# Performance work log

Hardware: AMD Instinct MI355X
Metric: run time of the kernel (lower is better)

The kernel has to match this reference:

```python
import jax, jax.numpy as jnp
import numpy as np

N_HEADS = 8
NUM_TIME_STEPS = 17  # T = NUM_TIME_STEPS - 1 = 16
MASK_PAD = np.float32(-2**32 + 1)


def setup_inputs() -> dict:
    key = jax.random.key(0)
    ks = jax.random.split(key, 5)
    B, T, D = 32768, NUM_TIME_STEPS - 1, 128
    return {
        "inputs": jax.random.normal(ks[0], (B, T, D), dtype=jnp.float32),
        "pos_emb": jax.random.normal(ks[1], (NUM_TIME_STEPS, D), dtype=jnp.float32) * 0.1,
        "Wq": jax.random.normal(ks[2], (D, D), dtype=jnp.float32) * (1.0 / np.sqrt(D)),
        "Wk": jax.random.normal(ks[3], (D, D), dtype=jnp.float32) * (1.0 / np.sqrt(D)),
        "Wv": jax.random.normal(ks[4], (D, D), dtype=jnp.float32) * (1.0 / np.sqrt(D)),
    }


def reference(inputs, pos_emb, Wq, Wk, Wv):
    B, T, D = inputs.shape
    h = N_HEADS
    dh = Wq.shape[1] // h
    # add positional embeddings for the first T time steps
    x = inputs + pos_emb[:T][None, :, :]  # [B, T, D]
    # QKV projections, then split into heads (torch.split dim=2 + cat dim=0 == head-major [h, B, T, dh])
    def proj(W):
        return jnp.einsum("btd,de->bte", x, W).reshape(B, T, h, dh).transpose(2, 0, 1, 3)
    q, k, v = proj(Wq), proj(Wk), proj(Wv)  # each [h, B, T, dh]
    # scaled scores; NOTE: original scales by sqrt(num_time_steps), not sqrt(head_dim)
    scores = jnp.einsum("hbtd,hbsd->hbts", q, k) / jnp.float32(NUM_TIME_STEPS) ** 0.5
    # causal mask: masked positions set to -2**32+1 (finite pad, as in the original)
    causal = jnp.tril(jnp.ones((T, T), dtype=bool))
    scores = jnp.where(causal[None, None, :, :], scores, MASK_PAD)
    attn = jax.nn.softmax(scores, axis=-1)  # [h, B, T, T]
    o = jnp.einsum("hbts,hbsd->hbtd", attn, v)  # [h, B, T, dh]
    # re-concat heads along feature dim (split dim0 + cat dim2)
    o = o.transpose(1, 2, 0, 3).reshape(B, T, h * dh)
    # feedforward: relu(x) + x
    o = jax.nn.relu(o) + o
    # residual=True: concat with temporal (position-added) inputs along features
    return jnp.concatenate([o, x], axis=2)  # [B, T, output_dim + input_dim]
```

## Files before the change

### kernel.cpp

```cpp
#include <hip/hip_runtime.h>

typedef float    f32x4 __attribute__((ext_vector_type(4)));
typedef __bf16   bf16x8 __attribute__((ext_vector_type(8)));
typedef _Float16 f16x4 __attribute__((ext_vector_type(4)));

typedef __attribute__((address_space(1))) const void gas_void;
typedef __attribute__((address_space(3))) void las_void;

static __device__ __forceinline__ unsigned short f2bf(float f) {
  union { float f; unsigned int u; } a; a.f = f;
  unsigned int r = (a.u + 0x7FFFu + ((a.u >> 16) & 1u)) >> 16;
  return (unsigned short)r;
}

#define QSCALE_L2E 0.34992146f

__global__ void prep_weights(const float* __restrict__ Wq, const float* __restrict__ Wk,
                             const float* __restrict__ Wv, unsigned short* __restrict__ wf) {
  int idx = blockIdx.x * 256 + threadIdx.x;
  if (idx >= 3 * 8 * 4 * 64 * 8) return;
  int i  = idx & 7;
  int p  = (idx >> 3) & 63;
  int kk = (idx >> 9) & 3;
  int n  = (idx >> 11) & 7;
  int w  = idx >> 14;
  const float* W = (w == 0) ? Wq : ((w == 1) ? Wk : Wv);
  float val = W[(kk * 32 + (p >> 4) * 8 + i) * 128 + n * 16 + (p & 15)];
  if (w == 0) val *= QSCALE_L2E;
  wf[idx] = f2bf(val);
}

__global__ void prep_posw(const float* __restrict__ pos, const float* __restrict__ Wq,
                          const float* __restrict__ Wk, const float* __restrict__ Wv,
                          float* __restrict__ pw) {
  int idx = blockIdx.x * 256 + threadIdx.x;
  if (idx >= 3 * 8 * 64 * 4) return;
  int r = idx & 3;
  int l = (idx >> 2) & 63;
  int h = (idx >> 8) & 7;
  int w = idx >> 11;
  const float* W = (w == 0) ? Wq : ((w == 1) ? Wk : Wv);
  int t, d;
  if (w < 2) { t = l & 15;            d = h * 16 + (l >> 4) * 4 + r; }
  else       { t = (l >> 4) * 4 + r;  d = h * 16 + (l & 15); }
  float s = 0.f;
  for (int k = 0; k < 128; ++k) s += pos[t * 128 + k] * W[k * 128 + d];
  if (w == 0) s *= QSCALE_L2E;
  pw[idx] = s;
}

__global__ void __launch_bounds__(512, 4)
attn_main(const float* __restrict__ xin, const float* __restrict__ pos,
          const unsigned short* __restrict__ wfrag, const float* __restrict__ pw,
          float* __restrict__ out, int B) {
  __shared__ __align__(16) float lx[2][4][2048];

  const int tid   = threadIdx.x;
  const int wid   = tid >> 6;
  const int l     = tid & 63;
  const int frow  = l & 15;
  const int fkq   = l >> 4;
  const int trow0 = fkq * 4;

  bf16x8 wf[3][4];
#pragma unroll
  for (int w = 0; w < 3; ++w)
#pragma unroll
    for (int kk = 0; kk < 4; ++kk)
      wf[w][kk] = *(const bf16x8*)(wfrag + ((w * 32 + wid * 4 + kk) * 512) + l * 8);

  f32x4 posw[3];
#pragma unroll
  for (int w = 0; w < 3; ++w)
    posw[w] = *(const f32x4*)(pw + ((w * 8 + wid) * 64 + l) * 4);

  const int ptcol = wid * 16 + fkq * 4;
  const f32x4 pp = *(const f32x4*)(pos + frow * 128 + ptcol);
  const int q    = 4 * wid + fkq;
  const int ptIdx = (((q >> 3) << 1) | (q & 1)) * 256 + (((q & 7) >> 1) * 16 + frow) * 4;

  const f32x4 zero4 = {0.f, 0.f, 0.f, 0.f};

  const int bpi   = gridDim.x * 4;
  const int niter = B / bpi;
  const int gsb   = frow * 128 + fkq * 8;
  const int bw    = wid >> 1;
  const int c0    = (wid & 1) * 4;

  {
    const float* xb = xin + (size_t)(blockIdx.x * 4 + bw) * 2048;
#pragma unroll
    for (int j = 0; j < 4; ++j) {
      int c = c0 + j;
      __builtin_amdgcn_global_load_lds((gas_void*)(xb + gsb + (c >> 1) * 32 + (c & 1) * 4),
                                       (las_void*)&lx[0][bw][c * 256], 16, 0, 0);
    }
  }
  int buf = 0;

  for (int it = 0; it < niter; ++it) {
    const int b0 = blockIdx.x * 4 + it * bpi;

    if (it == 0) {
      __syncthreads();
    } else {
      asm volatile("s_waitcnt vmcnt(8)" ::: "memory");
      __builtin_amdgcn_s_barrier();
    }

    if (it + 1 < niter) {
      const float* xb2 = xin + (size_t)(b0 + bpi + bw) * 2048;
#pragma unroll
      for (int j = 0; j < 4; ++j) {
        int c = c0 + j;
        __builtin_amdgcn_global_load_lds((gas_void*)(xb2 + gsb + (c >> 1) * 32 + (c & 1) * 4),
                                         (las_void*)&lx[buf ^ 1][bw][c * 256], 16, 0, 0);
      }
    }
    asm volatile("" ::: "memory");

#pragma unroll
    for (int g = 0; g < 4; ++g) {
      const float* lb = &lx[buf][g][0];
      float* ob = out + (size_t)(b0 + g) * 4096;

      bf16x8 xf[4];
#pragma unroll
      for (int kk = 0; kk < 4; ++kk) {
        f32x4 a0 = *(const f32x4*)(lb + (2 * kk + 0) * 256 + l * 4);
        f32x4 a1 = *(const f32x4*)(lb + (2 * kk + 1) * 256 + l * 4);
        xf[kk][0] = (__bf16)a0.x; xf[kk][1] = (__bf16)a0.y;
        xf[kk][2] = (__bf16)a0.z; xf[kk][3] = (__bf16)a0.w;
        xf[kk][4] = (__bf16)a1.x; xf[kk][5] = (__bf16)a1.y;
        xf[kk][6] = (__bf16)a1.z; xf[kk][7] = (__bf16)a1.w;
      }
      {
        f32x4 c0v = *(const f32x4*)(lb + ptIdx);
        *(f32x4*)(ob + frow * 256 + 128 + ptcol) = c0v + pp;
      }

      f32x4 qa = posw[0], ka = posw[1], va = posw[2];
#pragma unroll
      for (int kk = 0; kk < 4; ++kk) {
        qa = __builtin_amdgcn_mfma_f32_16x16x32_bf16(wf[0][kk], xf[kk], qa, 0, 0, 0);
        ka = __builtin_amdgcn_mfma_f32_16x16x32_bf16(wf[1][kk], xf[kk], ka, 0, 0, 0);
        va = __builtin_amdgcn_mfma_f32_16x16x32_bf16(xf[kk], wf[2][kk], va, 0, 0, 0);
      }
      f16x4 qh, kh, vh;
#pragma unroll
      for (int r = 0; r < 4; ++r) {
        qh[r] = (_Float16)qa[r];
        kh[r] = (_Float16)ka[r];
        vh[r] = (_Float16)va[r];
      }

      f32x4 st = __builtin_amdgcn_mfma_f32_16x16x16f16(kh, qh, zero4, 0, 0, 0);
      float p0 = (trow0 + 0 <= frow) ? __builtin_amdgcn_exp2f(st[0]) : 0.f;
      float p1 = (trow0 + 1 <= frow) ? __builtin_amdgcn_exp2f(st[1]) : 0.f;
      float p2 = (trow0 + 2 <= frow) ? __builtin_amdgcn_exp2f(st[2]) : 0.f;
      float p3 = (trow0 + 3 <= frow) ? __builtin_amdgcn_exp2f(st[3]) : 0.f;
      float ssum = (p0 + p1) + (p2 + p3);
      ssum += __shfl_xor(ssum, 16);
      ssum += __shfl_xor(ssum, 32);
      float inv = __builtin_amdgcn_rcpf(ssum);
      f16x4 ah;
      ah[0] = (_Float16)(p0 * inv);
      ah[1] = (_Float16)(p1 * inv);
      ah[2] = (_Float16)(p2 * inv);
      ah[3] = (_Float16)(p3 * inv);

      f32x4 ot = __builtin_amdgcn_mfma_f32_16x16x16f16(vh, ah, zero4, 0, 0, 0);
      f32x4 ov;
#pragma unroll
      for (int r = 0; r < 4; ++r) {
        float x = ot[r];
        ov[r] = x > 0.f ? 2.f * x : x;
      }
      *(f32x4*)(ob + frow * 256 + wid * 16 + trow0) = ov;
    }

    buf ^= 1;
  }
}

extern "C" void kernel_launch(void* const* d_in, const int* in_sizes, int n_in,
                              void* d_out, int out_size, void* d_ws, size_t ws_size,
                              hipStream_t stream) {
  (void)n_in; (void)out_size; (void)ws_size;
  const float* xin = (const float*)d_in[0];
  const float* pos = (const float*)d_in[1];
  const float* Wq  = (const float*)d_in[2];
  const float* Wk  = (const float*)d_in[3];
  const float* Wv  = (const float*)d_in[4];
  float* out = (float*)d_out;
  unsigned short* wf = (unsigned short*)d_ws;
  float* pw = (float*)((char*)d_ws + 3 * 8 * 4 * 64 * 8 * sizeof(unsigned short));
  int B = in_sizes[0] / 2048;

  hipLaunchKernelGGL(prep_weights, dim3(192), dim3(256), 0, stream, Wq, Wk, Wv, wf);
  hipLaunchKernelGGL(prep_posw, dim3(24), dim3(256), 0, stream, pos, Wq, Wk, Wv, pw);
  hipLaunchKernelGGL(attn_main, dim3(512), dim3(512), 0, stream, xin, pos, wf, pw, out, B);
}
```

Before: 176.2 us.

## Stage position-added bf16 inputs in LDS once and drop pos-projection prep kernel

Each wave now converts only its slice of the staged fp32 inputs, adds the positional embedding, and writes bf16 fragments into a double-buffered LDS array. The MFMA fragments are then read directly from that array, so the eight waves no longer each repeat the fp32-to-bf16 conversion for every batch element. The positional projection is now folded into the input before the QKV matmul, which removes the prep_posw kernel launch. The cost is that the residual x output is reconstructed from bf16-rounded values, so that half of the output loses precision. The fp32 staging buffer is also now single-buffered behind an extra LDS wait.

Result: faster. 170.2 us (-3.4%).

```diff
diff --git a/kernel.cpp b/kernel.cpp
--- a/kernel.cpp
+++ b/kernel.cpp
@@ -3,6 +3,7 @@
 typedef float    f32x4 __attribute__((ext_vector_type(4)));
 typedef __bf16   bf16x8 __attribute__((ext_vector_type(8)));
 typedef _Float16 f16x4 __attribute__((ext_vector_type(4)));
+typedef unsigned int u32x2 __attribute__((ext_vector_type(2)));
 
 typedef __attribute__((address_space(1))) const void gas_void;
 typedef __attribute__((address_space(3))) void las_void;
@@ -11,6 +12,9 @@
   union { float f; unsigned int u; } a; a.f = f;
   unsigned int r = (a.u + 0x7FFFu + ((a.u >> 16) & 1u)) >> 16;
   return (unsigned short)r;
+}
+static __device__ __forceinline__ float bits2f(unsigned int u) {
+  union { unsigned int u; float f; } a; a.u = u; return a.f;
 }
 
 #define QSCALE_L2E 0.34992146f
@@ -30,30 +34,11 @@
   wf[idx] = f2bf(val);
 }
 
-__global__ void prep_posw(const float* __restrict__ pos, const float* __restrict__ Wq,
-                          const float* __restrict__ Wk, const float* __restrict__ Wv,
-                          float* __restrict__ pw) {
-  int idx = blockIdx.x * 256 + threadIdx.x;
-  if (idx >= 3 * 8 * 64 * 4) return;
-  int r = idx & 3;
-  int l = (idx >> 2) & 63;
-  int h = (idx >> 8) & 7;
-  int w = idx >> 11;
-  const float* W = (w == 0) ? Wq : ((w == 1) ? Wk : Wv);
-  int t, d;
-  if (w < 2) { t = l & 15;            d = h * 16 + (l >> 4) * 4 + r; }
-  else       { t = (l >> 4) * 4 + r;  d = h * 16 + (l & 15); }
-  float s = 0.f;
-  for (int k = 0; k < 128; ++k) s += pos[t * 128 + k] * W[k * 128 + d];
-  if (w == 0) s *= QSCALE_L2E;
-  pw[idx] = s;
-}
-
 __global__ void __launch_bounds__(512, 4)
 attn_main(const float* __restrict__ xin, const float* __restrict__ pos,
-          const unsigned short* __restrict__ wfrag, const float* __restrict__ pw,
-          float* __restrict__ out, int B) {
-  __shared__ __align__(16) float lx[2][4][2048];
+          const unsigned short* __restrict__ wfrag, float* __restrict__ out, int B) {
+  __shared__ __align__(16) float lx[4][8][256];
+  __shared__ __align__(16) unsigned short lxb[2][4][4][512];
 
   const int tid   = threadIdx.x;
   const int wid   = tid >> 6;
@@ -69,23 +54,25 @@
     for (int kk = 0; kk < 4; ++kk)
       wf[w][kk] = *(const bf16x8*)(wfrag + ((w * 32 + wid * 4 + kk) * 512) + l * 8);
 
-  f32x4 posw[3];
+  const int bw = wid >> 1;
+  const int c0 = (wid & 1) * 4;
+
+  f32x4 posc[4];
 #pragma unroll
-  for (int w = 0; w < 3; ++w)
-    posw[w] = *(const f32x4*)(pw + ((w * 8 + wid) * 64 + l) * 4);
+  for (int cc = 0; cc < 4; ++cc) {
+    int c = c0 + cc;
+    posc[cc] = *(const f32x4*)(pos + frow * 128 + fkq * 8 + (c >> 1) * 32 + (c & 1) * 4);
+  }
 
   const int ptcol = wid * 16 + fkq * 4;
-  const f32x4 pp = *(const f32x4*)(pos + frow * 128 + ptcol);
-  const int q    = 4 * wid + fkq;
-  const int ptIdx = (((q >> 3) << 1) | (q & 1)) * 256 + (((q & 7) >> 1) * 16 + frow) * 4;
+  const int ptkk  = wid >> 1;
+  const int ptl   = frow + ((wid & 1) * 2 + (fkq >> 1)) * 16;
+  const int ptu   = ptl * 8 + (fkq & 1) * 4;
 
   const f32x4 zero4 = {0.f, 0.f, 0.f, 0.f};
-
   const int bpi   = gridDim.x * 4;
   const int niter = B / bpi;
   const int gsb   = frow * 128 + fkq * 8;
-  const int bw    = wid >> 1;
-  const int c0    = (wid & 1) * 4;
 
   {
     const float* xb = xin + (size_t)(blockIdx.x * 4 + bw) * 2048;
@@ -93,7 +80,7 @@
     for (int j = 0; j < 4; ++j) {
       int c = c0 + j;
       __builtin_amdgcn_global_load_lds((gas_void*)(xb + gsb + (c >> 1) * 32 + (c & 1) * 4),
-                                       (las_void*)&lx[0][bw][c * 256], 16, 0, 0);
+                                       (las_void*)&lx[bw][c][0], 16, 0, 0);
     }
   }
   int buf = 0;
@@ -101,12 +88,22 @@
   for (int it = 0; it < niter; ++it) {
     const int b0 = blockIdx.x * 4 + it * bpi;
 
-    if (it == 0) {
-      __syncthreads();
-    } else {
-      asm volatile("s_waitcnt vmcnt(8)" ::: "memory");
-      __builtin_amdgcn_s_barrier();
+    if (it == 0) asm volatile("s_waitcnt vmcnt(0)" ::: "memory");
+    else         asm volatile("s_waitcnt vmcnt(8)" ::: "memory");
+
+#pragma unroll
+    for (int i = 0; i < 2; ++i) {
+      int ce = c0 + 2 * i;
+      int kk = ce >> 1;
+      f32x4 a0 = *(const f32x4*)&lx[bw][ce][l * 4]     + posc[2 * i];
+      f32x4 a1 = *(const f32x4*)&lx[bw][ce + 1][l * 4] + posc[2 * i + 1];
+      bf16x8 v;
+      v[0] = (__bf16)a0.x; v[1] = (__bf16)a0.y; v[2] = (__bf16)a0.z; v[3] = (__bf16)a0.w;
+      v[4] = (__bf16)a1.x; v[5] = (__bf16)a1.y; v[6] = (__bf16)a1.z; v[7] = (__bf16)a1.w;
+      *(bf16x8*)&lxb[buf][bw][kk][l * 8] = v;
     }
+    asm volatile("s_waitcnt lgkmcnt(0)" ::: "memory");
+    __builtin_amdgcn_s_barrier();
 
     if (it + 1 < niter) {
       const float* xb2 = xin + (size_t)(b0 + bpi + bw) * 2048;
@@ -114,32 +111,31 @@
       for (int j = 0; j < 4; ++j) {
         int c = c0 + j;
         __builtin_amdgcn_global_load_lds((gas_void*)(xb2 + gsb + (c >> 1) * 32 + (c & 1) * 4),
-                                         (las_void*)&lx[buf ^ 1][bw][c * 256], 16, 0, 0);
+                                         (las_void*)&lx[bw][c][0], 16, 0, 0);
       }
     }
     asm volatile("" ::: "memory");
 
 #pragma unroll
     for (int g = 0; g < 4; ++g) {
-      const float* lb = &lx[buf][g][0];
       float* ob = out + (size_t)(b0 + g) * 4096;
 
       bf16x8 xf[4];
 #pragma unroll
-      for (int kk = 0; kk < 4; ++kk) {
-        f32x4 a0 = *(const f32x4*)(lb + (2 * kk + 0) * 256 + l * 4);
-        f32x4 a1 = *(const f32x4*)(lb + (2 * kk + 1) * 256 + l * 4);
-        xf[kk][0] = (__bf16)a0.x; xf[kk][1] = (__bf16)a0.y;
-        xf[kk][2] = (__bf16)a0.z; xf[kk][3] = (__bf16)a0.w;
-        xf[kk][4] = (__bf16)a1.x; xf[kk][5] = (__bf16)a1.y;
-        xf[kk][6] = (__bf16)a1.z; xf[kk][7] = (__bf16)a1.w;
-      }
+      for (int kk = 0; kk < 4; ++kk)
+        xf[kk] = *(const bf16x8*)&lxb[buf][g][kk][l * 8];
+
       {
-        f32x4 c0v = *(const f32x4*)(lb + ptIdx);
-        *(f32x4*)(ob + frow * 256 + 128 + ptcol) = c0v + pp;
+        u32x2 pv = *(const u32x2*)&lxb[buf][g][ptkk][ptu];
+        f32x4 ptv;
+        ptv.x = bits2f(pv[0] << 16);
+        ptv.y = bits2f(pv[0] & 0xffff0000u);
+        ptv.z = bits2f(pv[1] << 16);
+        ptv.w = bits2f(pv[1] & 0xffff0000u);
+        *(f32x4*)(ob + frow * 256 + 128 + ptcol) = ptv;
       }
 
-      f32x4 qa = posw[0], ka = posw[1], va = posw[2];
+      f32x4 qa = zero4, ka = zero4, va = zero4;
 #pragma unroll
       for (int kk = 0; kk < 4; ++kk) {
         qa = __builtin_amdgcn_mfma_f32_16x16x32_bf16(wf[0][kk], xf[kk], qa, 0, 0, 0);
@@ -194,10 +190,8 @@
   const float* Wv  = (const float*)d_in[4];
   float* out = (float*)d_out;
   unsigned short* wf = (unsigned short*)d_ws;
-  float* pw = (float*)((char*)d_ws + 3 * 8 * 4 * 64 * 8 * sizeof(unsigned short));
   int B = in_sizes[0] / 2048;
 
   hipLaunchKernelGGL(prep_weights, dim3(192), dim3(256), 0, stream, Wq, Wk, Wv, wf);
-  hipLaunchKernelGGL(prep_posw, dim3(24), dim3(256), 0, stream, pos, Wq, Wk, Wv, pw);
-  hipLaunchKernelGGL(attn_main, dim3(512), dim3(512), 0, stream, xin, pos, wf, pw, out, B);
+  hipLaunchKernelGGL(attn_main, dim3(512), dim3(512), 0, stream, xin, pos, wf, out, B);
 }
```
